# Performance work log

Hardware: AMD Instinct MI355X
Metric: run time of the kernel (lower is better)

Reference implementation:

```python
import jax, jax.numpy as jnp
import numpy as np

EMB_DIM = 1024
N_HEAD = 16
HEAD_DIM = EMB_DIM // N_HEAD  # 64
NUM_KV = 1
SEQ = 2048
BATCH = 2
QKV_OUT = (N_HEAD + 2 * NUM_KV) * HEAD_DIM  # 1152
ROPE_THETA = 10000.0


def _rope_tables(seq_len, dim):
    inv_freq = 1.0 / (ROPE_THETA ** (jnp.arange(0, dim, 2, dtype=jnp.float32) / dim))  # [dim/2]
    pos = jnp.arange(seq_len, dtype=jnp.float32)
    ang = pos[:, None] * inv_freq[None, :]  # [S, dim/2]
    return jnp.cos(ang), jnp.sin(ang)


def _apply_rope(x, cos, sin):
    # x: [B, S, H, D]; interleaved-pair rotation (torchtune-style)
    B, S, H, D = x.shape
    xr = x.reshape(B, S, H, D // 2, 2)
    x1, x2 = xr[..., 0], xr[..., 1]
    c = cos[None, :, None, :]
    s = sin[None, :, None, :]
    o1 = x1 * c - x2 * s
    o2 = x1 * s + x2 * c
    return jnp.stack([o1, o2], axis=-1).reshape(B, S, H, D)


def setup_inputs() -> dict:
    key = jax.random.key(0)
    k1, k2, k3, k4, k5 = jax.random.split(key, 5)
    scale = 1.0 / np.sqrt(EMB_DIM)
    return {
        "x": jax.random.normal(k1, (BATCH, SEQ, EMB_DIM), dtype=jnp.float32),
        "qkv_w": jax.random.uniform(k2, (QKV_OUT, EMB_DIM), jnp.float32, -scale, scale),
        "qkv_b": jax.random.uniform(k3, (QKV_OUT,), jnp.float32, -scale, scale),
        "out_w": jax.random.uniform(k4, (EMB_DIM, EMB_DIM), jnp.float32, -scale, scale),
        "out_b": jax.random.uniform(k5, (EMB_DIM,), jnp.float32, -scale, scale),
    }


def reference(x, qkv_w, qkv_b, out_w, out_b):
    B, S, E = x.shape
    qkv = x @ qkv_w.T + qkv_b  # [B, S, 1152]
    q_size = N_HEAD * HEAD_DIM
    kv_size = NUM_KV * HEAD_DIM
    q = qkv[..., :q_size].reshape(B, S, N_HEAD, HEAD_DIM)
    k = qkv[..., q_size:q_size + kv_size].reshape(B, S, NUM_KV, HEAD_DIM)
    v = qkv[..., q_size + kv_size:].reshape(B, S, NUM_KV, HEAD_DIM)

    cos, sin = _rope_tables(S, HEAD_DIM)
    q = _apply_rope(q, cos, sin)
    k = _apply_rope(k, cos, sin)

    q = q.transpose(0, 2, 1, 3)  # [B, H, S, D]
    k = k.transpose(0, 2, 1, 3)  # [B, 1, S, D]
    v = v.transpose(0, 2, 1, 3)  # [B, 1, S, D]

    # MQA: single KV head broadcasts over N_HEAD query heads
    scores = jnp.matmul(q, jnp.swapaxes(k, -2, -1)) / np.sqrt(HEAD_DIM)  # [B,H,S,S]
    causal = jnp.tril(jnp.ones((S, S), dtype=bool))
    scores = jnp.where(causal[None, None, :, :], scores, -jnp.inf)
    attn = jax.nn.softmax(scores, axis=-1)
    out = jnp.matmul(attn, v)  # [B, H, S, D]
    out = out.transpose(0, 2, 1, 3).reshape(B, S, E)
    return out @ out_w.T + out_b
```

## Files before the change

kernel.cpp:

```cpp
#include <hip/hip_runtime.h>
#include <stdint.h>
#include <stddef.h>

#define SEQ   2048
#define EMB   1024
#define NHEAD 16
#define HDIM  64
#define QKVO  1152
#define MTOT  4096

typedef __attribute__((ext_vector_type(4))) float f32x4;
typedef __attribute__((ext_vector_type(8))) short short8;
typedef __attribute__((ext_vector_type(4))) short s16x4;

__device__ __forceinline__ short f2bf(float f) {
  union { float f; unsigned u; } v; v.f = f;
  unsigned r = v.u + 0x7FFFu + ((v.u >> 16) & 1u);
  return (short)(r >> 16);
}

__device__ __forceinline__ unsigned cvtpk_bf16(float lo, float hi) {
  unsigned r;
  asm("v_cvt_pk_bf16_f32 %0, %1, %2" : "=v"(r) : "v"(lo), "v"(hi));
  return r;
}

__device__ __forceinline__ void gload16(const void* g, void* l) {
  __builtin_amdgcn_global_load_lds((const __attribute__((address_space(1))) void*)g,
                                   (__attribute__((address_space(3))) void*)l,
                                   16, 0, 0);
}

#define PX   524288
#define PW1  671744
#define PW2  802816
#define PTOT 811008

__device__ __forceinline__ void cvt8(const float* __restrict__ s, short* __restrict__ d) {
  float4 a = ((const float4*)s)[0];
  float4 b = ((const float4*)s)[1];
  short8 r;
  r[0]=f2bf(a.x); r[1]=f2bf(a.y); r[2]=f2bf(a.z); r[3]=f2bf(a.w);
  r[4]=f2bf(b.x); r[5]=f2bf(b.y); r[6]=f2bf(b.z); r[7]=f2bf(b.w);
  *(short8*)d = r;
}

__global__ __launch_bounds__(256) void prep_kernel(
    const float* __restrict__ x, const float* __restrict__ wqkv, const float* __restrict__ wout,
    short* __restrict__ xb, short* __restrict__ wqkvb, short* __restrict__ woutb,
    float* __restrict__ cost, float* __restrict__ sint) {
  int c = blockIdx.x * 256 + threadIdx.x;
  if (c < PX) {
    cvt8(x + (size_t)c * 8, xb + (size_t)c * 8);
  } else if (c < PW1) {
    int c2 = c - PX;
    cvt8(wqkv + (size_t)c2 * 8, wqkvb + (size_t)c2 * 8);
  } else if (c < PW2) {
    int c2 = c - PW1;
    cvt8(wout + (size_t)c2 * 8, woutb + (size_t)c2 * 8);
  } else if (c < PTOT) {
    int c2 = c - PW2;
    #pragma unroll
    for (int t = 0; t < 8; ++t) {
      int idx = c2 * 8 + t;
      int pos = idx >> 5, i = idx & 31;
      float inv = powf(10000.0f, -(float)i * (1.0f / 32.0f));
      float ang = (float)pos * inv;
      float sv, cv;
      sincosf(ang, &sv, &cv);
      cost[idx] = cv; sint[idx] = sv;
    }
  }
}

__device__ __forceinline__ void gstage64(
    const short* __restrict__ A, const short* __restrict__ Bm,
    int m0, int n0, int kt, short* buf, int tid) {
  #pragma unroll
  for (int rd = 0; rd < 2; ++rd) {
    const int ci = rd * 256 + tid;
    const int row = ci >> 3;
    const int sc = ((ci & 7) * 8) ^ ((row & 7) << 3);
    gload16(A  + (size_t)(m0 + row) * 1024 + kt + sc, buf + ci * 8);
    gload16(Bm + (size_t)(n0 + row) * 1024 + kt + sc, buf + 4096 + ci * 8);
  }
}

__device__ __forceinline__ void gemm_mainloop64(
    const short* __restrict__ A, const short* __restrict__ Bm,
    int m0, int n0, short* ls, f32x4 acc[2][2]) {
  const int tid = threadIdx.x, w = tid >> 6, lane = tid & 63;
  const int wm = w >> 1, wn = w & 1;
  const int lrow = lane & 15, lk = (lane >> 4) * 8;
  #pragma unroll
  for (int mi = 0; mi < 2; ++mi)
    #pragma unroll
    for (int ni = 0; ni < 2; ++ni)
      acc[mi][ni] = (f32x4){0.f, 0.f, 0.f, 0.f};
  const int rswz = (lrow & 7) << 3;

  gstage64(A, Bm, m0, n0, 0, ls, tid);
  for (int t = 0; t < 16; ++t) {
    short* cur = ls + (t & 1) * 8192;
    short* nxt = ls + ((t + 1) & 1) * 8192;
    if (t < 15) {
      gstage64(A, Bm, m0, n0, (t + 1) * 64, nxt, tid);
      asm volatile("s_waitcnt vmcnt(4)" ::: "memory");
    } else {
      asm volatile("s_waitcnt vmcnt(0)" ::: "memory");
    }
    __builtin_amdgcn_sched_barrier(0);
    __builtin_amdgcn_s_barrier();
    __builtin_amdgcn_sched_barrier(0);
    #pragma unroll
    for (int ks = 0; ks < 2; ++ks) {
      short8 af[2], bfv[2];
      #pragma unroll
      for (int mi = 0; mi < 2; ++mi) {
        const int row = wm * 32 + mi * 16 + lrow;
        af[mi] = *(const short8*)(cur + row * 64 + ((lk + ks * 32) ^ rswz));
      }
      #pragma unroll
      for (int ni = 0; ni < 2; ++ni) {
        const int row = wn * 32 + ni * 16 + lrow;
        bfv[ni] = *(const short8*)(cur + 4096 + row * 64 + ((lk + ks * 32) ^ rswz));
      }
      #pragma unroll
      for (int mi = 0; mi < 2; ++mi)
        #pragma unroll
        for (int ni = 0; ni < 2; ++ni)
          acc[mi][ni] = __builtin_amdgcn_mfma_f32_16x16x32_bf16(af[mi], bfv[ni], acc[mi][ni], 0, 0, 0);
    }
    __builtin_amdgcn_sched_barrier(0);
    __builtin_amdgcn_s_barrier();
  }
}

#define QSCALE 0.180336880111124f
#define QKV_NN 18

__global__ __launch_bounds__(256, 4) void qkv_kernel(
    const short* __restrict__ xb, const short* __restrict__ wb,
    const float* __restrict__ bias, const float* __restrict__ cost, const float* __restrict__ sint,
    short* __restrict__ qbuf, short* __restrict__ kbuf, short* __restrict__ vt) {
  __shared__ __align__(16) short ls[16384];
  f32x4 acc[2][2];
  const int nwg = 64 * QKV_NN;
  const int wg = (blockIdx.x & 7) * (nwg >> 3) + (blockIdx.x >> 3);
  const int m0 = (wg / QKV_NN) * 64, n0 = (wg % QKV_NN) * 64;
  gemm_mainloop64(xb, wb, m0, n0, ls, acc);

  const int w = threadIdx.x >> 6, lane = threadIdx.x & 63;
  const int wm = w >> 1, wn = w & 1;
  const int colb = n0 + wn * 32 + (lane & 15);
  const int rowb = m0 + wm * 32 + ((lane >> 4) << 2);
  #pragma unroll
  for (int ni = 0; ni < 2; ++ni) {
    const int col = colb + ni * 16;
    const float bv = bias[col];
    #pragma unroll
    for (int mi = 0; mi < 2; ++mi) {
      #pragma unroll
      for (int j = 0; j < 4; ++j) {
        const int m = rowb + mi * 16 + j;
        const int bb = m >> 11, pos = m & 2047;
        float v = acc[mi][ni][j] + bv;
        float vp = __shfl_xor(v, 1);
        float ov;
        if (col < 1088) {
          const int d = (col < 1024) ? (col & 63) : (col - 1024);
          const int i = d >> 1;
          const float cv = cost[pos * 32 + i], sv = sint[pos * 32 + i];
          ov = ((col & 1) == 0) ? (v * cv - vp * sv)
                                : (vp * sv + v * cv);
          if (col < 1024) ov *= QSCALE;
        } else {
          ov = v;
        }
        const short bfo = f2bf(ov);
        if (col < 1024) {
          const int h = col >> 6;
          qbuf[(((size_t)bb * NHEAD + h) * SEQ + pos) * HDIM + (col & 63)] = bfo;
        } else if (col < 1088) {
          kbuf[((size_t)bb * SEQ + pos) * HDIM + (col - 1024)] = bfo;
        } else {
          vt[((size_t)bb * HDIM + (col - 1088)) * SEQ + pos] = bfo;
        }
      }
    }
  }
}

template<bool MASKED>
__device__ __forceinline__ void attn_tile(
    const short* __restrict__ Kb, const short* __restrict__ Vb,
    int kv0, int qg, int g, int sadr0, int sadr1, int pswz,
    short* pls,
    short8 qf0, short8 qf1, float& m_run, float& l_run, f32x4 o[4]) {
  f32x4 st[4];
  __builtin_amdgcn_s_setprio(1);
  #pragma unroll
  for (int r = 0; r < 4; ++r) {
    short8 k0 = *(const short8*)(Kb + sadr0 + r * 1024);
    short8 k1 = *(const short8*)(Kb + sadr1 + r * 1024);
    f32x4 z = (f32x4){0.f, 0.f, 0.f, 0.f};
    z = __builtin_amdgcn_mfma_f32_16x16x32_bf16(k0, qf0, z, 0, 0, 0);
    z = __builtin_amdgcn_mfma_f32_16x16x32_bf16(k1, qf1, z, 0, 0, 0);
    st[r] = z;
  }
  __builtin_amdgcn_s_setprio(0);
  float s[16];
  #pragma unroll
  for (int r = 0; r < 4; ++r)
    #pragma unroll
    for (int j = 0; j < 4; ++j) {
      if (MASKED) {
        const int kv = kv0 + r * 16 + g * 4 + j;
        s[r * 4 + j] = (kv <= qg) ? st[r][j] : -1.0e38f;
      } else {
        s[r * 4 + j] = st[r][j];
      }
    }
  float a0 = fmaxf(fmaxf(s[0], s[1]), s[2]);
  float a1 = fmaxf(fmaxf(s[3], s[4]), s[5]);
  float a2 = fmaxf(fmaxf(s[6], s[7]), s[8]);
  float a3 = fmaxf(fmaxf(s[9], s[10]), s[11]);
  float a4 = fmaxf(fmaxf(s[12], s[13]), s[14]);
  float b0 = fmaxf(fmaxf(a0, a1), a2);
  float b1 = fmaxf(fmaxf(a3, a4), s[15]);
  float mt = fmaxf(b0, b1);
  mt = fmaxf(mt, __shfl_xor(mt, 16));
  mt = fmaxf(mt, __shfl_xor(mt, 32));
  if (!__all(mt <= m_run + 11.0f)) {
    const float m_new = fmaxf(m_run, mt);
    const float sc = __builtin_amdgcn_exp2f(m_run - m_new);
    #pragma unroll
    for (int nf = 0; nf < 4; ++nf) o[nf] *= sc;
    l_run *= sc;
    m_run = m_new;
  }
  float p[16], ps = 0.f;
  #pragma unroll
  for (int i = 0; i < 16; ++i) { p[i] = __builtin_amdgcn_exp2f(s[i] - m_run); ps += p[i]; }
  ps += __shfl_xor(ps, 16);
  ps += __shfl_xor(ps, 32);
  l_run += ps;
  #pragma unroll
  for (int r = 0; r < 4; ++r)
    #pragma unroll
    for (int jj = 0; jj < 4; jj += 2) {
      unsigned pk = cvtpk_bf16(p[r * 4 + jj], p[r * 4 + jj + 1]);
      *(unsigned*)(pls + ((r * 16 + g * 4 + jj) ^ pswz)) = pk;
    }
  short8 pb0 = *(const short8*)(pls + ((g * 8) ^ pswz));
  short8 pb1 = *(const short8*)(pls + ((32 + g * 8) ^ pswz));
  __builtin_amdgcn_s_setprio(1);
  #pragma unroll
  for (int nf = 0; nf < 4; ++nf) {
    short8 v0 = *(const short8*)(Vb + sadr0 + nf * 1024);
    short8 v1 = *(const short8*)(Vb + sadr1 + nf * 1024);
    o[nf] = __builtin_amdgcn_mfma_f32_16x16x32_bf16(v0, pb0, o[nf], 0, 0, 0);
    o[nf] = __builtin_amdgcn_mfma_f32_16x16x32_bf16(v1, pb1, o[nf], 0, 0, 0);
  }
  __builtin_amdgcn_s_setprio(0);
}

__device__ __forceinline__ void stage_kv(
    const short* __restrict__ kb_b, const short* __restrict__ vt_b, int kv0,
    short* Kb, short* Vb, int tid) {
  #pragma unroll
  for (int rd = 0; rd < 2; ++rd) {
    const int ci = rd * 256 + tid;
    const int r = ci >> 3;
    const int cs = ((ci & 7) * 8) ^ ((r & 7) << 3);
    gload16(kb_b + (size_t)(kv0 + r) * HDIM + cs, Kb + ci * 8);
  }
  #pragma unroll
  for (int rd = 0; rd < 2; ++rd) {
    const int ci = rd * 256 + tid;
    const int r = ci >> 3;
    const int cs = ((ci & 7) * 8) ^ ((r & 7) << 3);
    gload16(vt_b + (size_t)r * SEQ + kv0 + cs, Vb + ci * 8);
  }
}

__global__ __launch_bounds__(256, 4) void attn_kernel(
    const short* __restrict__ qb, const short* __restrict__ kb,
    const short* __restrict__ vt, short* __restrict__ ao) {
  __shared__ __align__(16) short Kls[2][4096];
  __shared__ __align__(16) short Vls[2][4096];
  __shared__ __align__(16) short plds[4][16][64];
  const int tid = threadIdx.x, w = tid >> 6, lane = tid & 63;
  const int bh = blockIdx.x, bb = bh >> 4, h = bh & 15;
  const int yy = blockIdx.y, kk = yy >> 3, bq = yy & 7;
  const int qchunk = (kk == 0) ? bq : (kk == 1) ? (15 - bq)
                   : (kk == 2) ? (16 + bq) : (31 - bq);
  const int q0 = qchunk * 64 + w * 16;
  const int g = lane >> 4, qloc = lane & 15;
  const int qg = q0 + qloc;

  const short* kb_b = kb + (size_t)bb * SEQ * HDIM;
  const short* vt_b = vt + (size_t)bb * HDIM * SEQ;

  const short* qbase = qb + (((size_t)bb * NHEAD + h) * SEQ + q0 + qloc) * HDIM + g * 8;
  short8 qf0 = *(const short8*)qbase;
  short8 qf1 = *(const short8*)(qbase + 32);

  f32x4 o[4];
  #pragma unroll
  for (int nf = 0; nf < 4; ++nf) o[nf] = (f32x4){0.f, 0.f, 0.f, 0.f};
  float m_run = -1.0e38f, l_run = 0.0f;

  short* pls = &plds[w][qloc][0];
  const int pswz = (qloc & 7) << 3;
  const int swm = (qloc & 7) << 3;
  const int sadr0 = qloc * 64 + ((g * 8) ^ swm);
  const int sadr1 = qloc * 64 + ((g * 8 + 32) ^ swm);

  stage_kv(kb_b, vt_b, 0, Kls[0], Vls[0], tid);
  const int nt = qchunk + 1;
  for (int t = 0; t < nt; ++t) {
    if (t + 1 < nt) {
      stage_kv(kb_b, vt_b, (t + 1) * 64, Kls[(t + 1) & 1], Vls[(t + 1) & 1], tid);
      asm volatile("s_waitcnt vmcnt(4)" ::: "memory");
    } else {
      asm volatile("s_waitcnt vmcnt(0)" ::: "memory");
    }
    __builtin_amdgcn_sched_barrier(0);
    __builtin_amdgcn_s_barrier();
    __builtin_amdgcn_sched_barrier(0);
    const short* Kb = Kls[t & 1];
    const short* Vb = Vls[t & 1];
    if (t + 1 < nt)
      attn_tile<false>(Kb, Vb, t * 64, qg, g, sadr0, sadr1, pswz, pls, qf0, qf1, m_run, l_run, o);
    else
      attn_tile<true>(Kb, Vb, t * 64, qg, g, sadr0, sadr1, pswz, pls, qf0, qf1, m_run, l_run, o);
    __builtin_amdgcn_sched_barrier(0);
    __builtin_amdgcn_s_barrier();
  }

  const float inv = 1.0f / l_run;
  const size_t obase = ((size_t)bb * SEQ + q0 + qloc) * EMB + (size_t)h * HDIM + g * 4;
  #pragma unroll
  for (int nf = 0; nf < 4; ++nf) {
    s16x4 pk;
    #pragma unroll
    for (int j = 0; j < 4; ++j) pk[j] = f2bf(o[nf][j] * inv);
    *(s16x4*)(ao + obase + nf * 16) = pk;
  }
}

#define OUT_NN 16

__global__ __launch_bounds__(256, 4) void out_kernel(
    const short* __restrict__ ab, const short* __restrict__ wb,
    const float* __restrict__ bias, float* __restrict__ out) {
  __shared__ __align__(16) short ls[16384];
  f32x4 acc[2][2];
  const int nwg = 64 * OUT_NN;
  const int wg = (blockIdx.x & 7) * (nwg >> 3) + (blockIdx.x >> 3);
  const int m0 = (wg >> 4) * 64, n0 = (wg & 15) * 64;
  gemm_mainloop64(ab, wb, m0, n0, ls, acc);

  const int w = threadIdx.x >> 6, lane = threadIdx.x & 63;
  const int wm = w >> 1, wn = w & 1;
  const int colb = n0 + wn * 32 + (lane & 15);
  const int rowb = m0 + wm * 32 + ((lane >> 4) << 2);
  #pragma unroll
  for (int ni = 0; ni < 2; ++ni) {
    const int col = colb + ni * 16;
    const float bv = bias[col];
    #pragma unroll
    for (int mi = 0; mi < 2; ++mi)
      #pragma unroll
      for (int j = 0; j < 4; ++j) {
        const int m = rowb + mi * 16 + j;
        out[(size_t)m * EMB + col] = acc[mi][ni][j] + bv;
      }
  }
}

extern "C" void kernel_launch(void* const* d_in, const int* in_sizes, int n_in,
                              void* d_out, int out_size, void* d_ws, size_t ws_size,
                              hipStream_t stream) {
  const float* x    = (const float*)d_in[0];
  const float* qkvw = (const float*)d_in[1];
  const float* qkvb = (const float*)d_in[2];
  const float* outw = (const float*)d_in[3];
  const float* outb = (const float*)d_in[4];
  float* out = (float*)d_out;
  char* ws = (char*)d_ws;

  short* xb    = (short*)(ws + 0);
  short* wqkvb = (short*)(ws + 8388608);
  short* woutb = (short*)(ws + 10747904);
  float* cost  = (float*)(ws + 12845056);
  float* sint  = (float*)(ws + 13107200);
  short* qbuf  = (short*)(ws + 13369344);
  short* kbuf  = (short*)(ws + 21757952);
  short* vtb   = (short*)(ws + 22282240);
  short* aob   = xb;

  prep_kernel<<<3168, 256, 0, stream>>>(x, qkvw, outw, xb, wqkvb, woutb, cost, sint);
  qkv_kernel<<<1152, 256, 0, stream>>>(xb, wqkvb, qkvb, cost, sint, qbuf, kbuf, vtb);
  attn_kernel<<<dim3(32, 32), 256, 0, stream>>>(qbuf, kbuf, vtb, aob);
  out_kernel<<<1024, 256, 0, stream>>>(aob, woutb, outb, out);
}
```

Measured before the change: 160.1 us.

## Run projection GEMM tiles with a single wave per workgroup, no barriers

The QKV and output projection GEMMs now launch one 64-thread wave per 64x64 tile instead of four waves. That single wave computes the whole tile with a 4x4 MFMA accumulator block and does all global-to-LDS staging itself. Because only one wave touches the LDS buffers, the s_barrier workgroup syncs are removed. The cost is fewer waves per tile, more registers per wave and more serial load issue per wave, which may reduce latency hiding and occupancy, since each workgroup still allocates 32KB of LDS.

```diff
diff --git a/kernel.cpp b/kernel.cpp
--- a/kernel.cpp
+++ b/kernel.cpp
@@ -73,93 +73,90 @@
   }
 }
 
-__device__ __forceinline__ void gstage64(
+__device__ __forceinline__ void gstage_w(
     const short* __restrict__ A, const short* __restrict__ Bm,
     int m0, int n0, int kt, short* buf, int tid) {
   #pragma unroll
-  for (int rd = 0; rd < 2; ++rd) {
-    const int ci = rd * 256 + tid;
+  for (int rd = 0; rd < 8; ++rd) {
+    const int ci = rd * 64 + tid;
     const int row = ci >> 3;
     const int sc = ((ci & 7) * 8) ^ ((row & 7) << 3);
-    gload16(A  + (size_t)(m0 + row) * 1024 + kt + sc, buf + ci * 8);
+    gload16(A + (size_t)(m0 + row) * 1024 + kt + sc, buf + ci * 8);
+  }
+  #pragma unroll
+  for (int rd = 0; rd < 8; ++rd) {
+    const int ci = rd * 64 + tid;
+    const int row = ci >> 3;
+    const int sc = ((ci & 7) * 8) ^ ((row & 7) << 3);
     gload16(Bm + (size_t)(n0 + row) * 1024 + kt + sc, buf + 4096 + ci * 8);
   }
 }
 
-__device__ __forceinline__ void gemm_mainloop64(
+__device__ __forceinline__ void gemm_wave(
     const short* __restrict__ A, const short* __restrict__ Bm,
-    int m0, int n0, short* ls, f32x4 acc[2][2]) {
-  const int tid = threadIdx.x, w = tid >> 6, lane = tid & 63;
-  const int wm = w >> 1, wn = w & 1;
-  const int lrow = lane & 15, lk = (lane >> 4) * 8;
-  #pragma unroll
-  for (int mi = 0; mi < 2; ++mi)
-    #pragma unroll
-    for (int ni = 0; ni < 2; ++ni)
+    int m0, int n0, short* ls, f32x4 acc[4][4]) {
+  const int tid = threadIdx.x;
+  const int lrow = tid & 15, lk = (tid >> 4) * 8;
+  const int rswz = (lrow & 7) << 3;
+  #pragma unroll
+  for (int mi = 0; mi < 4; ++mi)
+    #pragma unroll
+    for (int ni = 0; ni < 4; ++ni)
       acc[mi][ni] = (f32x4){0.f, 0.f, 0.f, 0.f};
-  const int rswz = (lrow & 7) << 3;
-
-  gstage64(A, Bm, m0, n0, 0, ls, tid);
+
+  gstage_w(A, Bm, m0, n0, 0, ls, tid);
   for (int t = 0; t < 16; ++t) {
     short* cur = ls + (t & 1) * 8192;
     short* nxt = ls + ((t + 1) & 1) * 8192;
+    __builtin_amdgcn_sched_barrier(0);
     if (t < 15) {
-      gstage64(A, Bm, m0, n0, (t + 1) * 64, nxt, tid);
-      asm volatile("s_waitcnt vmcnt(4)" ::: "memory");
+      gstage_w(A, Bm, m0, n0, (t + 1) * 64, nxt, tid);
+      asm volatile("s_waitcnt vmcnt(16)" ::: "memory");
     } else {
       asm volatile("s_waitcnt vmcnt(0)" ::: "memory");
     }
     __builtin_amdgcn_sched_barrier(0);
-    __builtin_amdgcn_s_barrier();
-    __builtin_amdgcn_sched_barrier(0);
     #pragma unroll
     for (int ks = 0; ks < 2; ++ks) {
-      short8 af[2], bfv[2];
+      short8 af[4], bfv[4];
       #pragma unroll
-      for (int mi = 0; mi < 2; ++mi) {
-        const int row = wm * 32 + mi * 16 + lrow;
-        af[mi] = *(const short8*)(cur + row * 64 + ((lk + ks * 32) ^ rswz));
-      }
+      for (int mi = 0; mi < 4; ++mi)
+        af[mi] = *(const short8*)(cur + (mi * 16 + lrow) * 64 + ((lk + ks * 32) ^ rswz));
       #pragma unroll
-      for (int ni = 0; ni < 2; ++ni) {
-        const int row = wn * 32 + ni * 16 + lrow;
-        bfv[ni] = *(const short8*)(cur + 4096 + row * 64 + ((lk + ks * 32) ^ rswz));
-      }
+      for (int ni = 0; ni < 4; ++ni)
+        bfv[ni] = *(const short8*)(cur + 4096 + (ni * 16 + lrow) * 64 + ((lk + ks * 32) ^ rswz));
       #pragma unroll
-      for (int mi = 0; mi < 2; ++mi)
+      for (int mi = 0; mi < 4; ++mi)
         #pragma unroll
-        for (int ni = 0; ni < 2; ++ni)
+        for (int ni = 0; ni < 4; ++ni)
           acc[mi][ni] = __builtin_amdgcn_mfma_f32_16x16x32_bf16(af[mi], bfv[ni], acc[mi][ni], 0, 0, 0);
     }
-    __builtin_amdgcn_sched_barrier(0);
-    __builtin_amdgcn_s_barrier();
   }
 }
 
 #define QSCALE 0.180336880111124f
 #define QKV_NN 18
 
-__global__ __launch_bounds__(256, 4) void qkv_kernel(
+__global__ __launch_bounds__(64) void qkv_kernel(
     const short* __restrict__ xb, const short* __restrict__ wb,
     const float* __restrict__ bias, const float* __restrict__ cost, const float* __restrict__ sint,
     short* __restrict__ qbuf, short* __restrict__ kbuf, short* __restrict__ vt) {
   __shared__ __align__(16) short ls[16384];
-  f32x4 acc[2][2];
+  f32x4 acc[4][4];
   const int nwg = 64 * QKV_NN;
   const int wg = (blockIdx.x & 7) * (nwg >> 3) + (blockIdx.x >> 3);
   const int m0 = (wg / QKV_NN) * 64, n0 = (wg % QKV_NN) * 64;
-  gemm_mainloop64(xb, wb, m0, n0, ls, acc);
-
-  const int w = threadIdx.x >> 6, lane = threadIdx.x & 63;
-  const int wm = w >> 1, wn = w & 1;
-  const int colb = n0 + wn * 32 + (lane & 15);
-  const int rowb = m0 + wm * 32 + ((lane >> 4) << 2);
-  #pragma unroll
-  for (int ni = 0; ni < 2; ++ni) {
-    const int col = colb + ni * 16;
+  gemm_wave(xb, wb, m0, n0, ls, acc);
+
+  const int tid = threadIdx.x;
+  const int lrow = tid & 15;
+  const int rowb = m0 + ((tid >> 4) << 2);
+  #pragma unroll
+  for (int ni = 0; ni < 4; ++ni) {
+    const int col = n0 + ni * 16 + lrow;
     const float bv = bias[col];
     #pragma unroll
-    for (int mi = 0; mi < 2; ++mi) {
+    for (int mi = 0; mi < 4; ++mi) {
       #pragma unroll
       for (int j = 0; j < 4; ++j) {
         const int m = rowb + mi * 16 + j;
@@ -352,26 +349,25 @@
 
 #define OUT_NN 16
 
-__global__ __launch_bounds__(256, 4) void out_kernel(
+__global__ __launch_bounds__(64) void out_kernel(
     const short* __restrict__ ab, const short* __restrict__ wb,
     const float* __restrict__ bias, float* __restrict__ out) {
   __shared__ __align__(16) short ls[16384];
-  f32x4 acc[2][2];
+  f32x4 acc[4][4];
   const int nwg = 64 * OUT_NN;
   const int wg = (blockIdx.x & 7) * (nwg >> 3) + (blockIdx.x >> 3);
   const int m0 = (wg >> 4) * 64, n0 = (wg & 15) * 64;
-  gemm_mainloop64(ab, wb, m0, n0, ls, acc);
-
-  const int w = threadIdx.x >> 6, lane = threadIdx.x & 63;
-  const int wm = w >> 1, wn = w & 1;
-  const int colb = n0 + wn * 32 + (lane & 15);
-  const int rowb = m0 + wm * 32 + ((lane >> 4) << 2);
-  #pragma unroll
-  for (int ni = 0; ni < 2; ++ni) {
-    const int col = colb + ni * 16;
+  gemm_wave(ab, wb, m0, n0, ls, acc);
+
+  const int tid = threadIdx.x;
+  const int lrow = tid & 15;
+  const int rowb = m0 + ((tid >> 4) << 2);
+  #pragma unroll
+  for (int ni = 0; ni < 4; ++ni) {
+    const int col = n0 + ni * 16 + lrow;
     const float bv = bias[col];
     #pragma unroll
-    for (int mi = 0; mi < 2; ++mi)
+    for (int mi = 0; mi < 4; ++mi)
       #pragma unroll
       for (int j = 0; j < 4; ++j) {
         const int m = rowb + mi * 16 + j;
@@ -402,7 +398,7 @@
   short* aob   = xb;
 
   prep_kernel<<<3168, 256, 0, stream>>>(x, qkvw, outw, xb, wqkvb, woutb, cost, sint);
-  qkv_kernel<<<1152, 256, 0, stream>>>(xb, wqkvb, qkvb, cost, sint, qbuf, kbuf, vtb);
+  qkv_kernel<<<1152, 64, 0, stream>>>(xb, wqkvb, qkvb, cost, sint, qbuf, kbuf, vtb);
   attn_kernel<<<dim3(32, 32), 256, 0, stream>>>(qbuf, kbuf, vtb, aob);
-  out_kernel<<<1024, 256, 0, stream>>>(aob, woutb, outb, out);
-}
+  out_kernel<<<1024, 64, 0, stream>>>(aob, woutb, outb, out);
+}
```

After: 190.6 us. 1.19x slower.
